# Optimization experiments

Hardware: AMD Instinct MI355X
Metric: run time of the kernel (lower is better)

## Reference

```python
import jax, jax.numpy as jnp
import numpy as np

N, K, CIN, COUT = 150000, 27, 128, 128


def setup_inputs() -> dict:
    key = jax.random.key(0)
    k1, k2, k3 = jax.random.split(key, 3)
    data = jax.random.normal(k1, (N, CIN), dtype=jnp.float32)
    weights = jax.random.normal(k2, (COUT, K, CIN), dtype=jnp.float32) * 0.05
    # neighbour indices in [-1, N): -1 marks empty octree neighbours (~1/151 here)
    neighbour = jax.random.randint(k3, (N, K), 0, N + 1, dtype=jnp.int64) - 1
    return {"data": data, "weights": weights, "neighbour": neighbour}


def reference(data, weights, neighbour):
    """Octree sparse conv: out[m] = sum_k W[:,k,:] @ data[neigh[m,k]] (0 if -1).

    Scans over the 27 kernel offsets so the [N,K,Cin] gather is never
    materialized; each step is a masked row-gather + dense GEMM.
    """
    w_k = jnp.transpose(weights, (1, 2, 0))   # [K, Cin, Cout]
    n_k = neighbour.T                          # [K, N]

    def body(acc, xs):
        w, idx = xs                            # [Cin, Cout], [N]
        valid = (idx >= 0)[:, None]            # [N, 1]
        g = jnp.where(valid, data[jnp.clip(idx, 0, None)], 0.0)  # [N, Cin]
        return acc + g @ w, None

    out0 = jnp.zeros((data.shape[0], w_k.shape[-1]), dtype=data.dtype)
    out, _ = jax.lax.scan(body, out0, (w_k, n_k))
    return out
```

## Files before the change

### kernel.cpp

```cpp
#include <hip/hip_runtime.h>

#define N_PTS 150000
#define NK 27
#define CIN 128
#define COUT 128
#define BM 256
#define NBLK ((N_PTS + BM - 1) / BM)

typedef __attribute__((ext_vector_type(8))) short bfrag8;
typedef __attribute__((ext_vector_type(4))) float facc4;

__device__ inline unsigned short f2bf(float f) {
    unsigned u = __builtin_bit_cast(unsigned, f);
    u += 0x7FFFu + ((u >> 16) & 1u);
    return (unsigned short)(u >> 16);
}
__device__ inline unsigned pack2(float a, float b) {
    return (unsigned)f2bf(a) | ((unsigned)f2bf(b) << 16);
}
__device__ inline void glds16(const void* g, void* l) {
    __builtin_amdgcn_global_load_lds(
        (const __attribute__((address_space(1))) void*)g,
        (__attribute__((address_space(3))) void*)l, 16, 0, 0);
}

__global__ void cast_data_kernel(const float* __restrict__ in,
                                 unsigned short* __restrict__ out) {
    const int n8_data = N_PTS * (CIN / 8);
    const int n8_all  = (N_PTS + 1) * (CIN / 8);
    int i = blockIdx.x * blockDim.x + threadIdx.x;
    int stride = gridDim.x * blockDim.x;
    for (; i < n8_all; i += stride) {
        uint4 v;
        if (i < n8_data) {
            const float4* p = (const float4*)(in + (size_t)i * 8);
            float4 x = p[0], y = p[1];
            v.x = pack2(x.x, x.y); v.y = pack2(x.z, x.w);
            v.z = pack2(y.x, y.y); v.w = pack2(y.z, y.w);
        } else {
            v.x = v.y = v.z = v.w = 0u;
        }
        *(uint4*)(out + (size_t)i * 8) = v;
    }
}

__global__ void prep_weights_h(const float* __restrict__ w,
                               unsigned short* __restrict__ wkh) {
    int i = blockIdx.x * blockDim.x + threadIdx.x;
    if (i >= NK * 2 * 128 * 8) return;
    int bu = i & 7, co = (i >> 3) & 127, h = (i >> 10) & 1, k = i >> 11;
    int ci = h * 64 + (bu ^ (co & 7)) * 8;
    const float4* src = (const float4*)(w + ((size_t)co * NK + k) * CIN + ci);
    float4 x = src[0], y = src[1];
    uint4 v;
    v.x = pack2(x.x, x.y); v.y = pack2(x.z, x.w);
    v.z = pack2(y.x, y.y); v.w = pack2(y.z, y.w);
    ((uint4*)wkh)[i] = v;
}


#define STAGE_A(Q, ADST)                                                     \
  {                                                                          \
    const int k_  = (Q) >> 1;                                                \
    const int hb_ = ((Q) & 1) << 7;                                          \
    int iv0 = *(const int*)(ldsI + s0 * 108 + k_ * 4);                       \
    int iv1 = *(const int*)(ldsI + s1 * 108 + k_ * 4);                       \
    int iv2 = *(const int*)(ldsI + s2 * 108 + k_ * 4);                       \
    int iv3 = *(const int*)(ldsI + s3 * 108 + k_ * 4);                       \
    size_t e0 = (s0ok && iv0 >= 0) ? (size_t)iv0 : (size_t)N_PTS;            \
    size_t e1 = (s1ok && iv1 >= 0) ? (size_t)iv1 : (size_t)N_PTS;            \
    size_t e2 = (s2ok && iv2 >= 0) ? (size_t)iv2 : (size_t)N_PTS;            \
    size_t e3 = (s3ok && iv3 >= 0) ? (size_t)iv3 : (size_t)N_PTS;            \
    glds16(dbfB + e0 * 256 + hb_ + aswz, (ADST) + s0 * 128 + lu16);          \
    glds16(dbfB + e1 * 256 + hb_ + aswz, (ADST) + s1 * 128 + lu16);          \
    glds16(dbfB + e2 * 256 + hb_ + aswz, (ADST) + s2 * 128 + lu16);          \
    glds16(dbfB + e3 * 256 + hb_ + aswz, (ADST) + s3 * 128 + lu16);          \
  }

#define STAGE_B(Q, BDST)                                                     \
  {                                                                          \
    const char* bs_ = wkhB + (size_t)(Q) * 16384 + t * 16;                   \
    glds16(bs_,        (BDST) + t * 16);                                     \
    glds16(bs_ + 8192, (BDST) + t * 16 + 8192);                              \
  }

#define MFMA_PHASE(ABUF, BBUF)                                                      \
  {                                                                                 \
    __builtin_amdgcn_s_setprio(1);                                                  \
    _Pragma("unroll")                                                               \
    for (int kk = 0; kk < 2; ++kk) {                                                \
      const int sw_ = (((kk * 4 + lk) ^ (lr & 7)) << 4);                            \
      bfrag8 a0 = *(const bfrag8*)((ABUF) + (wrow * 64 + lr) * 128 + sw_);          \
      bfrag8 a1 = *(const bfrag8*)((ABUF) + (wrow * 64 + 16 + lr) * 128 + sw_);     \
      bfrag8 a2 = *(const bfrag8*)((ABUF) + (wrow * 64 + 32 + lr) * 128 + sw_);     \
      bfrag8 a3 = *(const bfrag8*)((ABUF) + (wrow * 64 + 48 + lr) * 128 + sw_);     \
      _Pragma("unroll")                                                             \
      for (int ct = 0; ct < 4; ++ct) {                                              \
        bfrag8 b = *(const bfrag8*)((BBUF) + (h * 64 + ct * 16 + lr) * 128 + sw_);  \
        acc[0][ct] = __builtin_amdgcn_mfma_f32_16x16x32_bf16(a0, b, acc[0][ct],     \
                                                             0, 0, 0);              \
        acc[1][ct] = __builtin_amdgcn_mfma_f32_16x16x32_bf16(a1, b, acc[1][ct],     \
                                                             0, 0, 0);              \
        acc[2][ct] = __builtin_amdgcn_mfma_f32_16x16x32_bf16(a2, b, acc[2][ct],     \
                                                             0, 0, 0);              \
        acc[3][ct] = __builtin_amdgcn_mfma_f32_16x16x32_bf16(a3, b, acc[3][ct],     \
                                                             0, 0, 0);              \
      }                                                                             \
    }                                                                               \
    __builtin_amdgcn_s_setprio(0);                                                  \
  }

#define WAIT_BAR(N)                                                          \
    __builtin_amdgcn_sched_barrier(0);                                       \
    asm volatile("s_waitcnt vmcnt(" #N ")" ::: "memory");                    \
    __builtin_amdgcn_s_barrier();                                            \
    __builtin_amdgcn_sched_barrier(0);

__global__ __launch_bounds__(512, 2)
void octconv_v9(const unsigned short* __restrict__ dbf,
                const unsigned short* __restrict__ wkh,
                const int* __restrict__ nbr,
                float* __restrict__ out) {
    __shared__ __align__(1024) unsigned char lds[3 * 32768 + 2 * 16384 + 27648];

    const int t = threadIdx.x;
    const int w = t >> 6, l = t & 63;
    const int lr = l & 15, lk = l >> 4;
    const int h = w & 1, wrow = w >> 1;
    const int m0 = blockIdx.x * BM;

    const int lu   = l & 7;
    const int lu16 = lu * 16;
    const int sb   = w * 8 + (l >> 3);
    const int s0 = sb, s1 = sb + 64, s2 = sb + 128, s3 = sb + 192;
    const bool s0ok = (m0 + s0) < N_PTS;
    const bool s1ok = (m0 + s1) < N_PTS;
    const bool s2ok = (m0 + s2) < N_PTS;
    const bool s3ok = (m0 + s3) < N_PTS;
    const int aswz = (lu ^ (sb & 7)) << 4;

    const char* dbfB = (const char*)dbf;
    const char* wkhB = (const char*)wkh;
    char* a0p = (char*)lds;
    char* a1p = (char*)lds + 32768;
    char* a2p = (char*)lds + 65536;
    char* b0p = (char*)lds + 98304;
    char* b1p = (char*)lds + 114688;
    char* ldsI = (char*)lds + 131072;

    facc4 acc[4][4];
    const facc4 fz = {0.f, 0.f, 0.f, 0.f};
#pragma unroll
    for (int a = 0; a < 4; ++a)
#pragma unroll
        for (int b = 0; b < 4; ++b) acc[a][b] = fz;

    {
        const char* nsrc = (const char*)nbr + (size_t)m0 * 108;
        const int rows_valid = (N_PTS - m0) < BM ? (N_PTS - m0) : BM;
        const int nlimit = rows_valid * 108;
        int o;
        o = t * 16;         if (o < nlimit) glds16(nsrc + o, ldsI + o);
        o = 8192 + t * 16;  if (o < nlimit) glds16(nsrc + o, ldsI + o);
        o = 16384 + t * 16; if (o < nlimit) glds16(nsrc + o, ldsI + o);
        o = 24576 + t * 16; if (t < 192 && o < nlimit) glds16(nsrc + o, ldsI + o);
    }
    WAIT_BAR(0)

    STAGE_A(0, a0p)
    STAGE_B(0, b0p)
    STAGE_A(1, a1p)
    STAGE_B(1, b1p)
    WAIT_BAR(6)

    STAGE_A(2, a2p)
    MFMA_PHASE(a0p, b0p)
    WAIT_BAR(4)
    { char* tp = a0p; a0p = a1p; a1p = a2p; a2p = tp; }
    { char* tp = b0p; b0p = b1p; b1p = tp; }

#pragma unroll 1
    for (int p = 1; p <= 51; ++p) {
        STAGE_B(p + 1, b1p)
        STAGE_A(p + 2, a2p)
        MFMA_PHASE(a0p, b0p)
        WAIT_BAR(4)
        { char* tp = a0p; a0p = a1p; a1p = a2p; a2p = tp; }
        { char* tp = b0p; b0p = b1p; b1p = tp; }
    }

    STAGE_B(53, b1p)
    MFMA_PHASE(a0p, b0p)
    WAIT_BAR(0)
    { char* tp = a0p; a0p = a1p; a1p = a2p; a2p = tp; }
    { char* tp = b0p; b0p = b1p; b1p = tp; }

    MFMA_PHASE(a0p, b0p)

#pragma unroll
    for (int rt = 0; rt < 4; ++rt) {
        const int r0 = m0 + wrow * 64 + rt * 16 + lk * 4;
#pragma unroll
        for (int ct = 0; ct < 4; ++ct) {
#pragma unroll
            for (int r = 0; r < 4; ++r) {
                int row = r0 + r;
                if (row < N_PTS)
                    out[(size_t)row * COUT + h * 64 + ct * 16 + lr] = acc[rt][ct][r];
            }
        }
    }
}

__global__ void naive_kernel(const float* __restrict__ data, const float* __restrict__ wgt,
                             const int* __restrict__ nbr, float* __restrict__ out) {
    int mm = blockIdx.x;
    int co = threadIdx.x;
    if (mm >= N_PTS) return;
    float acc = 0.f;
    for (int k = 0; k < NK; ++k) {
        int idx = nbr[mm * NK + k];
        if (idx < 0) continue;
        const float* d  = data + (size_t)idx * CIN;
        const float* wp = wgt + ((size_t)co * NK + k) * CIN;
        for (int ci = 0; ci < CIN; ++ci) acc += d[ci] * wp[ci];
    }
    out[(size_t)mm * COUT + co] = acc;
}

extern "C" void kernel_launch(void* const* d_in, const int* in_sizes, int n_in,
                              void* d_out, int out_size, void* d_ws, size_t ws_size,
                              hipStream_t stream) {
    const float* data = (const float*)d_in[0];
    const float* wgt  = (const float*)d_in[1];
    const int*   nbr  = (const int*)d_in[2];
    float*       out  = (float*)d_out;

    const size_t wk_bytes  = (size_t)NK * 2 * 128 * 8 * 16;
    const size_t dbf_bytes = (size_t)(N_PTS + 1) * CIN * 2;

    if (ws_size < wk_bytes + dbf_bytes) {
        naive_kernel<<<N_PTS, COUT, 0, stream>>>(data, wgt, nbr, out);
        return;
    }
    unsigned short* wkh = (unsigned short*)d_ws;
    unsigned short* dbf = (unsigned short*)((char*)d_ws + wk_bytes);

    prep_weights_h<<<(NK * 2 * 128 * 8 + 255) / 256, 256, 0, stream>>>(wgt, wkh);
    cast_data_kernel<<<2048, 256, 0, stream>>>(data, dbf);

    octconv_v9<<<NBLK, 512, 0, stream>>>(dbf, wkh, nbr, out);
}
```

Before: 204.5 us.

## Halve row tile to 128 and double-buffer for higher occupancy

Cuts the per-block row tile from 256 to 128 and drops the triple-buffered A stage for plain double buffering with a full drain at each step. Accumulators per thread halve and LDS per block shrinks to about 77KB, so launch bounds now ask for 4 blocks per CU instead of 2. The aim is to hide gather latency through more resident waves rather than deeper prefetch. In exchange, every 128 rows load the full weight slice, doubling weight traffic, and each step waits for all outstanding loads, which removes overlap inside a block.

After: 189.0 us. 1.08x faster.

```diff
diff --git a/kernel.cpp b/kernel.cpp
--- a/kernel.cpp
+++ b/kernel.cpp
@@ -4,7 +4,7 @@
 #define NK 27
 #define CIN 128
 #define COUT 128
-#define BM 256
+#define BM 128
 #define NBLK ((N_PTS + BM - 1) / BM)
 
 typedef __attribute__((ext_vector_type(8))) short bfrag8;
@@ -65,16 +65,10 @@
     const int hb_ = ((Q) & 1) << 7;                                          \
     int iv0 = *(const int*)(ldsI + s0 * 108 + k_ * 4);                       \
     int iv1 = *(const int*)(ldsI + s1 * 108 + k_ * 4);                       \
-    int iv2 = *(const int*)(ldsI + s2 * 108 + k_ * 4);                       \
-    int iv3 = *(const int*)(ldsI + s3 * 108 + k_ * 4);                       \
     size_t e0 = (s0ok && iv0 >= 0) ? (size_t)iv0 : (size_t)N_PTS;            \
     size_t e1 = (s1ok && iv1 >= 0) ? (size_t)iv1 : (size_t)N_PTS;            \
-    size_t e2 = (s2ok && iv2 >= 0) ? (size_t)iv2 : (size_t)N_PTS;            \
-    size_t e3 = (s3ok && iv3 >= 0) ? (size_t)iv3 : (size_t)N_PTS;            \
     glds16(dbfB + e0 * 256 + hb_ + aswz, (ADST) + s0 * 128 + lu16);          \
     glds16(dbfB + e1 * 256 + hb_ + aswz, (ADST) + s1 * 128 + lu16);          \
-    glds16(dbfB + e2 * 256 + hb_ + aswz, (ADST) + s2 * 128 + lu16);          \
-    glds16(dbfB + e3 * 256 + hb_ + aswz, (ADST) + s3 * 128 + lu16);          \
   }
 
 #define STAGE_B(Q, BDST)                                                     \
@@ -90,10 +84,8 @@
     _Pragma("unroll")                                                               \
     for (int kk = 0; kk < 2; ++kk) {                                                \
       const int sw_ = (((kk * 4 + lk) ^ (lr & 7)) << 4);                            \
-      bfrag8 a0 = *(const bfrag8*)((ABUF) + (wrow * 64 + lr) * 128 + sw_);          \
-      bfrag8 a1 = *(const bfrag8*)((ABUF) + (wrow * 64 + 16 + lr) * 128 + sw_);     \
-      bfrag8 a2 = *(const bfrag8*)((ABUF) + (wrow * 64 + 32 + lr) * 128 + sw_);     \
-      bfrag8 a3 = *(const bfrag8*)((ABUF) + (wrow * 64 + 48 + lr) * 128 + sw_);     \
+      bfrag8 a0 = *(const bfrag8*)((ABUF) + (wrow * 32 + lr) * 128 + sw_);          \
+      bfrag8 a1 = *(const bfrag8*)((ABUF) + (wrow * 32 + 16 + lr) * 128 + sw_);     \
       _Pragma("unroll")                                                             \
       for (int ct = 0; ct < 4; ++ct) {                                              \
         bfrag8 b = *(const bfrag8*)((BBUF) + (h * 64 + ct * 16 + lr) * 128 + sw_);  \
@@ -101,10 +93,6 @@
                                                              0, 0, 0);              \
         acc[1][ct] = __builtin_amdgcn_mfma_f32_16x16x32_bf16(a1, b, acc[1][ct],     \
                                                              0, 0, 0);              \
-        acc[2][ct] = __builtin_amdgcn_mfma_f32_16x16x32_bf16(a2, b, acc[2][ct],     \
-                                                             0, 0, 0);              \
-        acc[3][ct] = __builtin_amdgcn_mfma_f32_16x16x32_bf16(a3, b, acc[3][ct],     \
-                                                             0, 0, 0);              \
       }                                                                             \
     }                                                                               \
     __builtin_amdgcn_s_setprio(0);                                                  \
@@ -116,12 +104,12 @@
     __builtin_amdgcn_s_barrier();                                            \
     __builtin_amdgcn_sched_barrier(0);
 
-__global__ __launch_bounds__(512, 2)
-void octconv_v9(const unsigned short* __restrict__ dbf,
-                const unsigned short* __restrict__ wkh,
-                const int* __restrict__ nbr,
-                float* __restrict__ out) {
-    __shared__ __align__(1024) unsigned char lds[3 * 32768 + 2 * 16384 + 27648];
+__global__ __launch_bounds__(512, 4)
+void octconv_v10(const unsigned short* __restrict__ dbf,
+                 const unsigned short* __restrict__ wkh,
+                 const int* __restrict__ nbr,
+                 float* __restrict__ out) {
+    __shared__ __align__(1024) unsigned char lds[2 * 16384 + 2 * 16384 + 13824];
 
     const int t = threadIdx.x;
     const int w = t >> 6, l = t & 63;
@@ -131,27 +119,24 @@
 
     const int lu   = l & 7;
     const int lu16 = lu * 16;
-    const int sb   = w * 8 + (l >> 3);
-    const int s0 = sb, s1 = sb + 64, s2 = sb + 128, s3 = sb + 192;
+    const int s0 = t >> 3;
+    const int s1 = s0 + 64;
     const bool s0ok = (m0 + s0) < N_PTS;
     const bool s1ok = (m0 + s1) < N_PTS;
-    const bool s2ok = (m0 + s2) < N_PTS;
-    const bool s3ok = (m0 + s3) < N_PTS;
-    const int aswz = (lu ^ (sb & 7)) << 4;
+    const int aswz = (lu ^ (s0 & 7)) << 4;
 
     const char* dbfB = (const char*)dbf;
     const char* wkhB = (const char*)wkh;
     char* a0p = (char*)lds;
-    char* a1p = (char*)lds + 32768;
-    char* a2p = (char*)lds + 65536;
-    char* b0p = (char*)lds + 98304;
-    char* b1p = (char*)lds + 114688;
-    char* ldsI = (char*)lds + 131072;
-
-    facc4 acc[4][4];
+    char* a1p = (char*)lds + 16384;
+    char* b0p = (char*)lds + 32768;
+    char* b1p = (char*)lds + 49152;
+    char* ldsI = (char*)lds + 65536;
+
+    facc4 acc[2][4];
     const facc4 fz = {0.f, 0.f, 0.f, 0.f};
 #pragma unroll
-    for (int a = 0; a < 4; ++a)
+    for (int a = 0; a < 2; ++a)
 #pragma unroll
         for (int b = 0; b < 4; ++b) acc[a][b] = fz;
 
@@ -160,46 +145,30 @@
         const int rows_valid = (N_PTS - m0) < BM ? (N_PTS - m0) : BM;
         const int nlimit = rows_valid * 108;
         int o;
-        o = t * 16;         if (o < nlimit) glds16(nsrc + o, ldsI + o);
-        o = 8192 + t * 16;  if (o < nlimit) glds16(nsrc + o, ldsI + o);
-        o = 16384 + t * 16; if (o < nlimit) glds16(nsrc + o, ldsI + o);
-        o = 24576 + t * 16; if (t < 192 && o < nlimit) glds16(nsrc + o, ldsI + o);
+        o = t * 16;        if (o < nlimit) glds16(nsrc + o, ldsI + o);
+        o = 8192 + t * 16; if (t < 352 && o < nlimit) glds16(nsrc + o, ldsI + o);
     }
     WAIT_BAR(0)
 
     STAGE_A(0, a0p)
     STAGE_B(0, b0p)
-    STAGE_A(1, a1p)
-    STAGE_B(1, b1p)
-    WAIT_BAR(6)
-
-    STAGE_A(2, a2p)
+    WAIT_BAR(0)
+
+#pragma unroll 1
+    for (int p = 0; p <= 52; ++p) {
+        STAGE_B(p + 1, b1p)
+        STAGE_A(p + 1, a1p)
+        MFMA_PHASE(a0p, b0p)
+        WAIT_BAR(0)
+        { char* tp = a0p; a0p = a1p; a1p = tp; }
+        { char* tp = b0p; b0p = b1p; b1p = tp; }
+    }
+
     MFMA_PHASE(a0p, b0p)
-    WAIT_BAR(4)
-    { char* tp = a0p; a0p = a1p; a1p = a2p; a2p = tp; }
-    { char* tp = b0p; b0p = b1p; b1p = tp; }
-
-#pragma unroll 1
-    for (int p = 1; p <= 51; ++p) {
-        STAGE_B(p + 1, b1p)
-        STAGE_A(p + 2, a2p)
-        MFMA_PHASE(a0p, b0p)
-        WAIT_BAR(4)
-        { char* tp = a0p; a0p = a1p; a1p = a2p; a2p = tp; }
-        { char* tp = b0p; b0p = b1p; b1p = tp; }
-    }
-
-    STAGE_B(53, b1p)
-    MFMA_PHASE(a0p, b0p)
-    WAIT_BAR(0)
-    { char* tp = a0p; a0p = a1p; a1p = a2p; a2p = tp; }
-    { char* tp = b0p; b0p = b1p; b1p = tp; }
-
-    MFMA_PHASE(a0p, b0p)
-
-#pragma unroll
-    for (int rt = 0; rt < 4; ++rt) {
-        const int r0 = m0 + wrow * 64 + rt * 16 + lk * 4;
+
+#pragma unroll
+    for (int rt = 0; rt < 2; ++rt) {
+        const int r0 = m0 + wrow * 32 + rt * 16 + lk * 4;
 #pragma unroll
         for (int ct = 0; ct < 4; ++ct) {
 #pragma unroll
@@ -249,5 +218,5 @@
     prep_weights_h<<<(NK * 2 * 128 * 8 + 255) / 256, 256, 0, stream>>>(wgt, wkh);
     cast_data_kernel<<<2048, 256, 0, stream>>>(data, dbf);
 
-    octconv_v9<<<NBLK, 512, 0, stream>>>(dbf, wkh, nbr, out);
-}
+    octconv_v10<<<NBLK, 512, 0, stream>>>(dbf, wkh, nbr, out);
+}
```
